# Optimization experiments

Measured on AMD Instinct MI355X. Metric: run time of the kernel, lower is better.

## Reference

```python
import jax, jax.numpy as jnp
import numpy as np

N_NODES = 50000
N_EDGES = 600000
IN_CH = 128
HID = 128
OUT_CH = 16
N_REL = 8
NEG_SLOPE = 0.2


def glorot(key, shape):
    fan_in, fan_out = shape[-2], shape[-1]
    lim = (6.0 / (fan_in + fan_out)) ** 0.5
    return jax.random.uniform(key, shape, jnp.float32, -lim, lim)


def setup_inputs() -> dict:
    key = jax.random.key(0)
    ks = jax.random.split(key, 16)
    x = jax.random.normal(ks[0], (N_NODES, IN_CH), jnp.float32)
    edge_index = jax.random.randint(ks[1], (2, N_EDGES), 0, N_NODES, jnp.int64)
    edge_type = jax.random.randint(ks[2], (N_EDGES,), 0, N_REL, jnp.int64)
    return {
        "x": x,
        "W1": glorot(ks[3], (N_REL, IN_CH, HID)),
        "q1": glorot(ks[4], (HID, 1)),
        "k1": glorot(ks[5], (HID, 1)),
        "b1": jnp.zeros((HID,), jnp.float32),
        "W2": glorot(ks[6], (N_REL, HID, HID)),
        "q2": glorot(ks[7], (HID, 1)),
        "k2": glorot(ks[8], (HID, 1)),
        "b2": jnp.zeros((HID,), jnp.float32),
        "lin_w": glorot(ks[9], (HID, OUT_CH)),
        "lin_b": jnp.zeros((OUT_CH,), jnp.float32),
        "edge_index": edge_index,
        "edge_type": edge_type,
    }


def rgat_conv(x, W, q, k, b, src, dst, etype, n_nodes):
    # Per-relation linear transform of all nodes: [R, N, H]
    xw = jnp.einsum('ni,rio->rno', x, W)
    hj = xw[etype, src]  # transformed source features per edge [E, H]
    hi = xw[etype, dst]  # transformed target features per edge [E, H]
    # additive self-attention logits (heads=1, dim=1): [E, 1]
    a = jax.nn.leaky_relu(hi @ q + hj @ k, NEG_SLOPE)
    # segment softmax over incoming edges of each target node (across-relation)
    amax = jax.ops.segment_max(a, dst, num_segments=n_nodes)  # [N, 1]
    e = jnp.exp(a - amax[dst])
    denom = jax.ops.segment_sum(e, dst, num_segments=n_nodes)  # [N, 1]
    alpha = e / denom[dst]
    # weighted scatter-add aggregation + bias
    out = jax.ops.segment_sum(alpha * hj, dst, num_segments=n_nodes)
    return out + b


def reference(x, W1, q1, k1, b1, W2, q2, k2, b2, lin_w, lin_b, edge_index, edge_type):
    src, dst = edge_index[0], edge_index[1]
    n = x.shape[0]
    h = jax.nn.relu(rgat_conv(x, W1, q1, k1, b1, src, dst, edge_type, n))
    h = jax.nn.relu(rgat_conv(h, W2, q2, k2, b2, src, dst, edge_type, n))
    h = h @ lin_w + lin_b                 # [N, out]
    g = jnp.mean(h, axis=0, keepdims=True)  # global_mean_pool -> [1, out]
    return jax.nn.log_softmax(g, axis=-1)
```

## Files before the change

kernel.cpp:

```cpp
#include <hip/hip_runtime.h>

#define CH 128
#define N_REL 8
#define OUT_CH 16
#define NEG_SLOPE 0.2f

typedef short short8 __attribute__((ext_vector_type(8)));
typedef float f32x4 __attribute__((ext_vector_type(4)));

__device__ __forceinline__ unsigned short f2bf(float f) {
    unsigned u = __float_as_uint(f);
    return (unsigned short)((u + 0x7fffu + ((u >> 16) & 1u)) >> 16);
}

__global__ void k_wqk(const float* __restrict__ W, const float* __restrict__ qv,
                      const float* __restrict__ kv, float* __restrict__ wq,
                      float* __restrict__ wk) {
    int r = blockIdx.x;
    int i = threadIdx.x;
    const float* row = W + ((size_t)r * CH + i) * CH;
    float aq = 0.f, ak = 0.f;
    for (int o = 0; o < CH; ++o) { float w = row[o]; aq += w * qv[o]; ak += w * kv[o]; }
    wq[r * CH + i] = aq;
    wk[r * CH + i] = ak;
}

__global__ void k_qkpack(const float* __restrict__ wq, const float* __restrict__ wk,
                         unsigned short* __restrict__ qkf) {
    int tid = threadIdx.x;
    int lane = tid & 63, ks = tid >> 6;
    int j = lane & 15, g = lane >> 4;
    const float* col = (j < 8) ? (wq + j * CH) : (wk + (j - 8) * CH);
    int k0 = ks * 32 + g * 8;
    unsigned pk[4];
    #pragma unroll
    for (int p = 0; p < 4; ++p) {
        unsigned lo = f2bf(col[k0 + 2 * p]);
        unsigned hi = f2bf(col[k0 + 2 * p + 1]);
        pk[p] = lo | (hi << 16);
    }
    *(uint4*)(qkf + (size_t)tid * 8) = make_uint4(pk[0], pk[1], pk[2], pk[3]);
}

__global__ __launch_bounds__(256) void k_sqsk2(const unsigned short* __restrict__ Xb,
                                               const unsigned short* __restrict__ qkf,
                                               float* __restrict__ sq,
                                               float* __restrict__ sk, int n) {
    const int wv = threadIdx.x >> 6, lane = threadIdx.x & 63;
    const int l15 = lane & 15, g = lane >> 4;
    const int t = blockIdx.x * 4 + wv;
    const int ntiles = (n + 15) >> 4;
    if (t >= ntiles) return;

    short8 qf[4];
    #pragma unroll
    for (int ks = 0; ks < 4; ++ks)
        qf[ks] = *(const short8*)(qkf + (size_t)(ks * 64 + lane) * 8);

    int row = t * 16 + l15;
    bool ok = row < n;
    int rowc = ok ? row : n - 1;
    const unsigned short* xrow = Xb + (size_t)rowc * CH + g * 8;
    short8 xf[4];
    #pragma unroll
    for (int ks = 0; ks < 4; ++ks) xf[ks] = *(const short8*)(xrow + ks * 32);

    f32x4 dq = {0.f, 0.f, 0.f, 0.f};
    #pragma unroll
    for (int ks = 0; ks < 4; ++ks)
        dq = __builtin_amdgcn_mfma_f32_16x16x32_bf16(qf[ks], xf[ks], dq, 0, 0, 0);

    if (ok) {
        float* base = (g < 2) ? sq : sk;
        int j0 = (g & 1) * 4;
        #pragma unroll
        for (int reg = 0; reg < 4; ++reg)
            base[(size_t)(j0 + reg) * n + row] = dq[reg];
    }
}

__global__ void k_cast(const float* __restrict__ X, unsigned short* __restrict__ Xb,
                       long total) {
    long i = ((long)blockIdx.x * 256 + threadIdx.x) * 8;
    if (i >= total) return;
    float4 v0 = *(const float4*)(X + i);
    float4 v1 = *(const float4*)(X + i + 4);
    ushort4 a, b;
    a.x = f2bf(v0.x); a.y = f2bf(v0.y); a.z = f2bf(v0.z); a.w = f2bf(v0.w);
    b.x = f2bf(v1.x); b.y = f2bf(v1.y); b.z = f2bf(v1.z); b.w = f2bf(v1.w);
    *(ushort4*)(Xb + i) = a;
    *(ushort4*)(Xb + i + 4) = b;
}

__global__ void k_wpack(const float* __restrict__ W, unsigned short* __restrict__ Wpk) {
    int t = blockIdx.x * 256 + threadIdx.x;
    if (t >= N_REL * 8 * 4 * 64) return;
    int lane = t & 63, ks = (t >> 6) & 3, ct = (t >> 8) & 7, r = t >> 11;
    int l15 = lane & 15, g = lane >> 4;
    const float* src = W + ((size_t)r * CH + ks * 32 + g * 8) * CH + ct * 16 + l15;
    unsigned pk[4];
    for (int p = 0; p < 4; ++p) {
        unsigned lo = f2bf(src[(2 * p) * CH]);
        unsigned hi = f2bf(src[(2 * p + 1) * CH]);
        pk[p] = lo | (hi << 16);
    }
    uint4 o = make_uint4(pk[0], pk[1], pk[2], pk[3]);
    *(uint4*)(Wpk + (size_t)t * 8) = o;
}

__global__ __launch_bounds__(256) void k_gemm3(const unsigned short* __restrict__ Xb,
                                               const unsigned short* __restrict__ Wpk,
                                               unsigned short* __restrict__ XW,
                                               int n, int nwaves) {
    const int wv = threadIdx.x >> 6, lane = threadIdx.x & 63;
    const int l15 = lane & 15, g = lane >> 4;
    const int w = blockIdx.x * 4 + wv;
    const int r = w & 7;
    const int slot = w >> 3;
    const int nslots = nwaves >> 3;
    const int ntiles = (n + 15) >> 4;

    short8 wf[8][4];
    const unsigned short* wr = Wpk + ((size_t)r * 32 * 64 + lane) * 8;
    #pragma unroll
    for (int ct = 0; ct < 8; ++ct)
        #pragma unroll
        for (int ks = 0; ks < 4; ++ks)
            wf[ct][ks] = *(const short8*)(wr + (size_t)(ct * 4 + ks) * 64 * 8);

    for (int t = slot; t < ntiles; t += nslots) {
        int row = t * 16 + l15;
        bool ok = row < n;
        int rowc = ok ? row : n - 1;
        const unsigned short* xrow = Xb + (size_t)rowc * CH + g * 8;
        short8 xf[4];
        #pragma unroll
        for (int ks = 0; ks < 4; ++ks) xf[ks] = *(const short8*)(xrow + ks * 32);
        unsigned short* orow = XW + ((size_t)r * n + row) * CH;
        #pragma unroll
        for (int ct = 0; ct < 8; ++ct) {
            f32x4 a = {0.f, 0.f, 0.f, 0.f};
            #pragma unroll
            for (int ks = 0; ks < 4; ++ks)
                a = __builtin_amdgcn_mfma_f32_16x16x32_bf16(wf[ct][ks], xf[ks], a, 0, 0, 0);
            unsigned p01, p23;
            asm("v_cvt_pk_bf16_f32 %0, %1, %2" : "=v"(p01) : "v"(a[0]), "v"(a[1]));
            asm("v_cvt_pk_bf16_f32 %0, %1, %2" : "=v"(p23) : "v"(a[2]), "v"(a[3]));
            if (ok) *(uint2*)(orow + ct * 16 + g * 4) = make_uint2(p01, p23);
        }
    }
}

__global__ void k_hist(const int* __restrict__ dst, int* __restrict__ count, int ne) {
    int e = blockIdx.x * 256 + threadIdx.x;
    if (e >= ne) return;
    atomicAdd(count + dst[e], 1);
}

__global__ __launch_bounds__(256) void k_scan1(const int* __restrict__ count,
                                               int* __restrict__ rowptr,
                                               int* __restrict__ bsum, int n) {
    __shared__ int wsum[4];
    int b = blockIdx.x, tid = threadIdx.x, lane = tid & 63, w = tid >> 6;
    int i0 = b * 1024 + tid * 4;
    int v0 = 0, v1 = 0, v2 = 0, v3 = 0;
    if (i0 + 3 < n) {
        int4 v = *(const int4*)(count + i0);
        v0 = v.x; v1 = v.y; v2 = v.z; v3 = v.w;
    } else {
        if (i0 < n) v0 = count[i0];
        if (i0 + 1 < n) v1 = count[i0 + 1];
        if (i0 + 2 < n) v2 = count[i0 + 2];
        if (i0 + 3 < n) v3 = count[i0 + 3];
    }
    int t1 = v0 + v1, t2 = t1 + v2, t3 = t2 + v3;
    int s = t3;
    #pragma unroll
    for (int off = 1; off < 64; off <<= 1) {
        int t = __shfl_up(s, off);
        if (lane >= off) s += t;
    }
    if (lane == 63) wsum[w] = s;
    __syncthreads();
    int wpre = 0;
    #pragma unroll
    for (int i = 0; i < 4; ++i) wpre += (i < w) ? wsum[i] : 0;
    int excl = wpre + s - t3;
    if (i0 < n) rowptr[i0] = excl;
    if (i0 + 1 < n) rowptr[i0 + 1] = excl + v0;
    if (i0 + 2 < n) rowptr[i0 + 2] = excl + t1;
    if (i0 + 3 < n) rowptr[i0 + 3] = excl + t2;
    if (tid == 0) bsum[b] = wsum[0] + wsum[1] + wsum[2] + wsum[3];
}

__global__ void k_scan2(int* __restrict__ bsum, int* __restrict__ total, int nb) {
    int lane = threadIdx.x;
    int carry = 0;
    for (int base = 0; base < nb; base += 64) {
        int i = base + lane;
        int v = (i < nb) ? bsum[i] : 0;
        int s = v;
        #pragma unroll
        for (int off = 1; off < 64; off <<= 1) {
            int t = __shfl_up(s, off);
            if (lane >= off) s += t;
        }
        if (i < nb) bsum[i] = carry + s - v;
        carry += __shfl(s, 63);
    }
    if (lane == 0) *total = carry;
}

__global__ __launch_bounds__(256) void k_scan3(int* __restrict__ rowptr,
                                               int* __restrict__ rowptr_work,
                                               const int* __restrict__ bsum,
                                               const int* __restrict__ total, int n) {
    int b = blockIdx.x;
    int i0 = b * 1024 + threadIdx.x * 4;
    int add = bsum[b];
    #pragma unroll
    for (int j = 0; j < 4; ++j) {
        int i = i0 + j;
        if (i < n) {
            int v = rowptr[i] + add;
            rowptr[i] = v;
            rowptr_work[i] = v;
        }
    }
    if (b == 0 && threadIdx.x == 0) rowptr[n] = *total;
}

__global__ void k_scatter(const int* __restrict__ src, const int* __restrict__ dst,
                          const int* __restrict__ et, int* __restrict__ rowptr_work,
                          int* __restrict__ pe, int ne) {
    int e = blockIdx.x * 256 + threadIdx.x;
    if (e >= ne) return;
    int pos = atomicAdd(rowptr_work + dst[e], 1);
    pe[pos] = (src[e] & 0xffff) | (et[e] << 16);
}

__global__ __launch_bounds__(256) void k_attn(
    const int* __restrict__ rowptr, const int* __restrict__ pe,
    const float* __restrict__ sq, const float* __restrict__ sk,
    const unsigned short* __restrict__ XW, const float* __restrict__ bias,
    unsigned short* __restrict__ outb, int n_nodes) {
    int wid = (blockIdx.x * 256 + threadIdx.x) >> 6;
    int lane = threadIdx.x & 63;
    if (wid >= n_nodes) return;
    const int l16 = lane & 15, g16 = lane >> 4;
    int r0 = rowptr[wid], r1 = rowptr[wid + 1];
    float acc[8] = {};
    float denom = 0.f;

    if (r1 > r0) {
        float sqv = (lane < N_REL) ? sq[lane * n_nodes + wid] : 0.f;

        float m = -1e30f;
        for (int c0 = r0; c0 < r1; c0 += 64) {
            int j = c0 + lane;
            float a = -1e30f;
            if (j < r1) {
                int p = pe[j];
                int s = p & 0xffff, t = p >> 16;
                float av = __shfl(sqv, t) + sk[t * n_nodes + s];
                a = av >= 0.f ? av : NEG_SLOPE * av;
            }
            m = fmaxf(m, a);
        }
        #pragma unroll
        for (int off = 32; off; off >>= 1) m = fmaxf(m, __shfl_xor(m, off));

        for (int c0 = r0; c0 < r1; c0 += 64) {
            int j = c0 + lane;
            float ev = 0.f;
            int p = 0;
            if (j < r1) {
                p = pe[j];
                int s = p & 0xffff, t = p >> 16;
                float av = __shfl(sqv, t) + sk[t * n_nodes + s];
                av = av >= 0.f ? av : NEG_SLOPE * av;
                ev = __expf(av - m);
            }
            float evs = ev;
            #pragma unroll
            for (int off = 32; off; off >>= 1) evs += __shfl_xor(evs, off);
            denom += evs;

            int C = r1 - c0;
            if (C > 64) C = 64;
            for (int jj = 0; jj < C; jj += 4) {
                int lsel = jj + g16;
                float evj = __shfl(ev, lsel);
                int pj = __shfl(p, lsel);
                int s = pj & 0xffff, t = pj >> 16;
                const unsigned short* row = XW + ((size_t)(t * n_nodes + s)) * CH + l16 * 8;
                uint4 v = *(const uint4*)row;
                acc[0] += evj * __uint_as_float(v.x << 16);
                acc[1] += evj * __uint_as_float(v.x & 0xffff0000u);
                acc[2] += evj * __uint_as_float(v.y << 16);
                acc[3] += evj * __uint_as_float(v.y & 0xffff0000u);
                acc[4] += evj * __uint_as_float(v.z << 16);
                acc[5] += evj * __uint_as_float(v.z & 0xffff0000u);
                acc[6] += evj * __uint_as_float(v.w << 16);
                acc[7] += evj * __uint_as_float(v.w & 0xffff0000u);
            }
        }
    }

    #pragma unroll
    for (int i = 0; i < 8; ++i) {
        acc[i] += __shfl_xor(acc[i], 16);
        acc[i] += __shfl_xor(acc[i], 32);
    }

    if (lane < 16) {
        float inv = denom > 0.f ? 1.f / denom : 0.f;
        unsigned pk[4];
        #pragma unroll
        for (int i = 0; i < 4; ++i) {
            float b0 = bias[l16 * 8 + 2 * i];
            float b1 = bias[l16 * 8 + 2 * i + 1];
            float o0 = acc[2 * i] * inv + b0;
            float o1 = acc[2 * i + 1] * inv + b1;
            o0 = o0 > 0.f ? o0 : 0.f;
            o1 = o1 > 0.f ? o1 : 0.f;
            pk[i] = (unsigned)f2bf(o0) | ((unsigned)f2bf(o1) << 16);
        }
        *(uint4*)(outb + (size_t)wid * CH + l16 * 8) = make_uint4(pk[0], pk[1], pk[2], pk[3]);
    }
}

__global__ __launch_bounds__(256) void k_colsum(const unsigned short* __restrict__ h,
                                                float* __restrict__ sum, int n_nodes) {
    __shared__ float cs[CH];
    int tid = threadIdx.x;
    int c2 = (tid & 63) * 2;
    int rw = tid >> 6;
    if (tid < CH) cs[tid] = 0.f;
    __syncthreads();
    float a0 = 0.f, a1 = 0.f;
    for (int row = blockIdx.x * 4 + rw; row < n_nodes; row += gridDim.x * 4) {
        unsigned v = *(const unsigned*)(h + (size_t)row * CH + c2);
        a0 += __uint_as_float(v << 16);
        a1 += __uint_as_float(v & 0xffff0000u);
    }
    atomicAdd(&cs[c2], a0);
    atomicAdd(&cs[c2 + 1], a1);
    __syncthreads();
    if (tid < CH) atomicAdd(sum + tid, cs[tid]);
}

__global__ void k_head(const float* __restrict__ sum, const float* __restrict__ lw,
                       const float* __restrict__ lb, float* __restrict__ outp, int n_nodes) {
    __shared__ float mean[CH];
    int t = threadIdx.x;
    mean[t] = sum[t] / (float)n_nodes;
    __syncthreads();
    if (t < OUT_CH) {
        float g = lb[t];
        for (int i = 0; i < CH; ++i) g += mean[i] * lw[i * OUT_CH + t];
        float m = g;
        #pragma unroll
        for (int off = 8; off; off >>= 1) m = fmaxf(m, __shfl_xor(m, off, 16));
        float ex = expf(g - m);
        float se = ex;
        #pragma unroll
        for (int off = 8; off; off >>= 1) se += __shfl_xor(se, off, 16);
        outp[t] = g - m - logf(se);
    }
}

extern "C" void kernel_launch(void* const* d_in, const int* in_sizes, int n_in,
                              void* d_out, int out_size, void* d_ws, size_t ws_size,
                              hipStream_t stream) {
    const float* x  = (const float*)d_in[0];
    const float* W1 = (const float*)d_in[1];
    const float* q1 = (const float*)d_in[2];
    const float* k1 = (const float*)d_in[3];
    const float* b1 = (const float*)d_in[4];
    const float* W2 = (const float*)d_in[5];
    const float* q2 = (const float*)d_in[6];
    const float* k2 = (const float*)d_in[7];
    const float* b2 = (const float*)d_in[8];
    const float* lw = (const float*)d_in[9];
    const float* lb = (const float*)d_in[10];
    const int* ei   = (const int*)d_in[11];
    const int* etp  = (const int*)d_in[12];

    const int n  = in_sizes[0] / CH;
    const int ne = in_sizes[12];
    const int* esrc = ei;
    const int* edst = ei + ne;

    char* ws = (char*)d_ws;
    size_t off = 0;
    auto carve = [&](size_t bytes) -> char* {
        char* p = ws + off;
        off = (off + bytes + 255) & ~(size_t)255;
        return p;
    };
    unsigned short* xw  = (unsigned short*)carve((size_t)N_REL * n * CH * 2);
    unsigned short* xb  = (unsigned short*)carve((size_t)n * CH * 2);
    unsigned short* h1b = (unsigned short*)carve((size_t)n * CH * 2);
    unsigned short* h2b = (unsigned short*)carve((size_t)n * CH * 2);
    unsigned short* wpk = (unsigned short*)carve((size_t)N_REL * 32 * 64 * 8 * 2);
    unsigned short* qkf = (unsigned short*)carve((size_t)256 * 8 * 2);
    float* sq     = (float*)carve((size_t)N_REL * n * 4);
    float* sk     = (float*)carve((size_t)N_REL * n * 4);
    float* wq     = (float*)carve(N_REL * CH * 4);
    float* wk     = (float*)carve(N_REL * CH * 4);
    int* count    = (int*)carve((size_t)n * 4);
    int* rowptr   = (int*)carve((size_t)(n + 1) * 4);
    int* rowptr_w = (int*)carve((size_t)n * 4);
    int* pe       = (int*)carve((size_t)ne * 4);
    int* bsum     = (int*)carve((size_t)256 * 4);
    int* total    = (int*)carve(4);
    float* sum128 = (float*)carve(CH * 4);

    hipMemsetAsync(count, 0, (size_t)n * 4, stream);
    hipMemsetAsync(sum128, 0, CH * 4, stream);

    const int nbscan = (n + 1023) / 1024;
    k_hist<<<(ne + 255) / 256, 256, 0, stream>>>(edst, count, ne);
    k_scan1<<<nbscan, 256, 0, stream>>>(count, rowptr, bsum, n);
    k_scan2<<<1, 64, 0, stream>>>(bsum, total, nbscan);
    k_scan3<<<nbscan, 256, 0, stream>>>(rowptr, rowptr_w, bsum, total, n);
    k_scatter<<<(ne + 255) / 256, 256, 0, stream>>>(esrc, edst, etp, rowptr_w, pe, ne);

    const int wpack_threads = N_REL * 8 * 4 * 64;
    const int NW = 2048;
    const int ntiles = (n + 15) >> 4;

    auto run_layer = [&](const unsigned short* Xb, const float* W, const float* qv,
                         const float* kv, const float* bv, unsigned short* houtb) {
        k_wqk<<<N_REL, CH, 0, stream>>>(W, qv, kv, wq, wk);
        k_wpack<<<(wpack_threads + 255) / 256, 256, 0, stream>>>(W, wpk);
        k_qkpack<<<1, 256, 0, stream>>>(wq, wk, qkf);
        k_gemm3<<<NW / 4, 256, 0, stream>>>(Xb, wpk, xw, n, NW);
        k_sqsk2<<<(ntiles + 3) / 4, 256, 0, stream>>>(Xb, qkf, sq, sk, n);
        k_attn<<<(n + 3) / 4, 256, 0, stream>>>(rowptr, pe, sq, sk, xw, bv, houtb, n);
    };

    k_cast<<<(int)(((long)n * CH / 8 + 255) / 256), 256, 0, stream>>>(x, xb, (long)n * CH);
    run_layer(xb, W1, q1, k1, b1, h1b);
    run_layer(h1b, W2, q2, k2, b2, h2b);

    k_colsum<<<256, 256, 0, stream>>>(h2b, sum128, n);
    k_head<<<1, CH, 0, stream>>>(sum128, lw, lb, (float*)d_out, n);
}
```

Baseline: 282.7 us.

## Horizontally fuse independent prep, scan, GEMM and scatter kernels into fewer launches

Independent kernels are merged into combined launches that pick their role from the block index: cast with histogram, scan1 with the first layer's W·q/W·k, scan2 with weight packing, and GEMM with the sq/sk projection and edge scatter. The second layer's W·q/W·k is also folded into the first layer's attention launch. This cuts the number of launches and the serialization gaps between small kernels, and lets small jobs overlap with large ones. The cost is more complex launch-dependency reasoning and mixed-role blocks that may raise register pressure or hurt occupancy in the fused kernels.

```diff
diff --git a/kernel.cpp b/kernel.cpp
--- a/kernel.cpp
+++ b/kernel.cpp
@@ -13,11 +13,28 @@
     return (unsigned short)((u + 0x7fffu + ((u >> 16) & 1u)) >> 16);
 }
 
-__global__ void k_wqk(const float* __restrict__ W, const float* __restrict__ qv,
-                      const float* __restrict__ kv, float* __restrict__ wq,
-                      float* __restrict__ wk) {
-    int r = blockIdx.x;
-    int i = threadIdx.x;
+
+__device__ __forceinline__ void dev_cast(const float* __restrict__ X,
+                                         unsigned short* __restrict__ Xb,
+                                         long total, int b, int tid) {
+    long i = ((long)b * 256 + tid) * 8;
+    if (i >= total) return;
+    float4 v0 = *(const float4*)(X + i);
+    float4 v1 = *(const float4*)(X + i + 4);
+    ushort4 a, c;
+    a.x = f2bf(v0.x); a.y = f2bf(v0.y); a.z = f2bf(v0.z); a.w = f2bf(v0.w);
+    c.x = f2bf(v1.x); c.y = f2bf(v1.y); c.z = f2bf(v1.z); c.w = f2bf(v1.w);
+    *(ushort4*)(Xb + i) = a;
+    *(ushort4*)(Xb + i + 4) = c;
+}
+
+__device__ __forceinline__ void dev_wqk(const float* __restrict__ W,
+                                        const float* __restrict__ qv,
+                                        const float* __restrict__ kv,
+                                        float* __restrict__ wq, float* __restrict__ wk,
+                                        int rb, int tid) {
+    int r = rb * 2 + (tid >> 7);
+    int i = tid & 127;
     const float* row = W + ((size_t)r * CH + i) * CH;
     float aq = 0.f, ak = 0.f;
     for (int o = 0; o < CH; ++o) { float w = row[o]; aq += w * qv[o]; ak += w * kv[o]; }
@@ -25,9 +42,24 @@
     wk[r * CH + i] = ak;
 }
 
-__global__ void k_qkpack(const float* __restrict__ wq, const float* __restrict__ wk,
-                         unsigned short* __restrict__ qkf) {
-    int tid = threadIdx.x;
+__device__ __forceinline__ void dev_wpack(const float* __restrict__ W,
+                                          unsigned short* __restrict__ Wpk, int t) {
+    int lane = t & 63, ks = (t >> 6) & 3, ct = (t >> 8) & 7, r = t >> 11;
+    int l15 = lane & 15, g = lane >> 4;
+    const float* src = W + ((size_t)r * CH + ks * 32 + g * 8) * CH + ct * 16 + l15;
+    unsigned pk[4];
+    #pragma unroll
+    for (int p = 0; p < 4; ++p) {
+        unsigned lo = f2bf(src[(2 * p) * CH]);
+        unsigned hi = f2bf(src[(2 * p + 1) * CH]);
+        pk[p] = lo | (hi << 16);
+    }
+    *(uint4*)(Wpk + (size_t)t * 8) = make_uint4(pk[0], pk[1], pk[2], pk[3]);
+}
+
+__device__ __forceinline__ void dev_qkpack(const float* __restrict__ wq,
+                                           const float* __restrict__ wk,
+                                           unsigned short* __restrict__ qkf, int tid) {
     int lane = tid & 63, ks = tid >> 6;
     int j = lane & 15, g = lane >> 4;
     const float* col = (j < 8) ? (wq + j * CH) : (wk + (j - 8) * CH);
@@ -42,126 +74,31 @@
     *(uint4*)(qkf + (size_t)tid * 8) = make_uint4(pk[0], pk[1], pk[2], pk[3]);
 }
 
-__global__ __launch_bounds__(256) void k_sqsk2(const unsigned short* __restrict__ Xb,
-                                               const unsigned short* __restrict__ qkf,
-                                               float* __restrict__ sq,
-                                               float* __restrict__ sk, int n) {
-    const int wv = threadIdx.x >> 6, lane = threadIdx.x & 63;
-    const int l15 = lane & 15, g = lane >> 4;
-    const int t = blockIdx.x * 4 + wv;
-    const int ntiles = (n + 15) >> 4;
-    if (t >= ntiles) return;
-
-    short8 qf[4];
-    #pragma unroll
-    for (int ks = 0; ks < 4; ++ks)
-        qf[ks] = *(const short8*)(qkf + (size_t)(ks * 64 + lane) * 8);
-
-    int row = t * 16 + l15;
-    bool ok = row < n;
-    int rowc = ok ? row : n - 1;
-    const unsigned short* xrow = Xb + (size_t)rowc * CH + g * 8;
-    short8 xf[4];
-    #pragma unroll
-    for (int ks = 0; ks < 4; ++ks) xf[ks] = *(const short8*)(xrow + ks * 32);
-
-    f32x4 dq = {0.f, 0.f, 0.f, 0.f};
-    #pragma unroll
-    for (int ks = 0; ks < 4; ++ks)
-        dq = __builtin_amdgcn_mfma_f32_16x16x32_bf16(qf[ks], xf[ks], dq, 0, 0, 0);
-
-    if (ok) {
-        float* base = (g < 2) ? sq : sk;
-        int j0 = (g & 1) * 4;
-        #pragma unroll
-        for (int reg = 0; reg < 4; ++reg)
-            base[(size_t)(j0 + reg) * n + row] = dq[reg];
-    }
-}
-
-__global__ void k_cast(const float* __restrict__ X, unsigned short* __restrict__ Xb,
-                       long total) {
-    long i = ((long)blockIdx.x * 256 + threadIdx.x) * 8;
-    if (i >= total) return;
-    float4 v0 = *(const float4*)(X + i);
-    float4 v1 = *(const float4*)(X + i + 4);
-    ushort4 a, b;
-    a.x = f2bf(v0.x); a.y = f2bf(v0.y); a.z = f2bf(v0.z); a.w = f2bf(v0.w);
-    b.x = f2bf(v1.x); b.y = f2bf(v1.y); b.z = f2bf(v1.z); b.w = f2bf(v1.w);
-    *(ushort4*)(Xb + i) = a;
-    *(ushort4*)(Xb + i + 4) = b;
-}
-
-__global__ void k_wpack(const float* __restrict__ W, unsigned short* __restrict__ Wpk) {
-    int t = blockIdx.x * 256 + threadIdx.x;
-    if (t >= N_REL * 8 * 4 * 64) return;
-    int lane = t & 63, ks = (t >> 6) & 3, ct = (t >> 8) & 7, r = t >> 11;
-    int l15 = lane & 15, g = lane >> 4;
-    const float* src = W + ((size_t)r * CH + ks * 32 + g * 8) * CH + ct * 16 + l15;
-    unsigned pk[4];
-    for (int p = 0; p < 4; ++p) {
-        unsigned lo = f2bf(src[(2 * p) * CH]);
-        unsigned hi = f2bf(src[(2 * p + 1) * CH]);
-        pk[p] = lo | (hi << 16);
-    }
-    uint4 o = make_uint4(pk[0], pk[1], pk[2], pk[3]);
-    *(uint4*)(Wpk + (size_t)t * 8) = o;
-}
-
-__global__ __launch_bounds__(256) void k_gemm3(const unsigned short* __restrict__ Xb,
-                                               const unsigned short* __restrict__ Wpk,
-                                               unsigned short* __restrict__ XW,
-                                               int n, int nwaves) {
-    const int wv = threadIdx.x >> 6, lane = threadIdx.x & 63;
-    const int l15 = lane & 15, g = lane >> 4;
-    const int w = blockIdx.x * 4 + wv;
-    const int r = w & 7;
-    const int slot = w >> 3;
-    const int nslots = nwaves >> 3;
-    const int ntiles = (n + 15) >> 4;
-
-    short8 wf[8][4];
-    const unsigned short* wr = Wpk + ((size_t)r * 32 * 64 + lane) * 8;
-    #pragma unroll
-    for (int ct = 0; ct < 8; ++ct)
-        #pragma unroll
-        for (int ks = 0; ks < 4; ++ks)
-            wf[ct][ks] = *(const short8*)(wr + (size_t)(ct * 4 + ks) * 64 * 8);
-
-    for (int t = slot; t < ntiles; t += nslots) {
-        int row = t * 16 + l15;
-        bool ok = row < n;
-        int rowc = ok ? row : n - 1;
-        const unsigned short* xrow = Xb + (size_t)rowc * CH + g * 8;
-        short8 xf[4];
-        #pragma unroll
-        for (int ks = 0; ks < 4; ++ks) xf[ks] = *(const short8*)(xrow + ks * 32);
-        unsigned short* orow = XW + ((size_t)r * n + row) * CH;
-        #pragma unroll
-        for (int ct = 0; ct < 8; ++ct) {
-            f32x4 a = {0.f, 0.f, 0.f, 0.f};
-            #pragma unroll
-            for (int ks = 0; ks < 4; ++ks)
-                a = __builtin_amdgcn_mfma_f32_16x16x32_bf16(wf[ct][ks], xf[ks], a, 0, 0, 0);
-            unsigned p01, p23;
-            asm("v_cvt_pk_bf16_f32 %0, %1, %2" : "=v"(p01) : "v"(a[0]), "v"(a[1]));
-            asm("v_cvt_pk_bf16_f32 %0, %1, %2" : "=v"(p23) : "v"(a[2]), "v"(a[3]));
-            if (ok) *(uint2*)(orow + ct * 16 + g * 4) = make_uint2(p01, p23);
-        }
-    }
-}
-
-__global__ void k_hist(const int* __restrict__ dst, int* __restrict__ count, int ne) {
-    int e = blockIdx.x * 256 + threadIdx.x;
-    if (e >= ne) return;
-    atomicAdd(count + dst[e], 1);
-}
-
-__global__ __launch_bounds__(256) void k_scan1(const int* __restrict__ count,
-                                               int* __restrict__ rowptr,
-                                               int* __restrict__ bsum, int n) {
+
+__global__ void k_cast_hist(const float* __restrict__ X, unsigned short* __restrict__ Xb,
+                            long total, const int* __restrict__ dst,
+                            int* __restrict__ count, int ne, int nb_cast) {
+    int b = blockIdx.x, tid = threadIdx.x;
+    if (b < nb_cast) {
+        dev_cast(X, Xb, total, b, tid);
+    } else {
+        int e = (b - nb_cast) * 256 + tid;
+        if (e < ne) atomicAdd(count + dst[e], 1);
+    }
+}
+
+__global__ __launch_bounds__(256) void k_scan1_wqk(const int* __restrict__ count,
+                                                   int* __restrict__ rowptr,
+                                                   int* __restrict__ bsum, int n, int nbscan,
+                                                   const float* __restrict__ W,
+                                                   const float* __restrict__ qv,
+                                                   const float* __restrict__ kv,
+                                                   float* __restrict__ wq,
+                                                   float* __restrict__ wk) {
+    int b = blockIdx.x, tid = threadIdx.x;
+    if (b >= nbscan) { dev_wqk(W, qv, kv, wq, wk, b - nbscan, tid); return; }
     __shared__ int wsum[4];
-    int b = blockIdx.x, tid = threadIdx.x, lane = tid & 63, w = tid >> 6;
+    int lane = tid & 63, w = tid >> 6;
     int i0 = b * 1024 + tid * 4;
     int v0 = 0, v1 = 0, v2 = 0, v3 = 0;
     if (i0 + 3 < n) {
@@ -193,22 +130,36 @@
     if (tid == 0) bsum[b] = wsum[0] + wsum[1] + wsum[2] + wsum[3];
 }
 
-__global__ void k_scan2(int* __restrict__ bsum, int* __restrict__ total, int nb) {
-    int lane = threadIdx.x;
-    int carry = 0;
-    for (int base = 0; base < nb; base += 64) {
-        int i = base + lane;
-        int v = (i < nb) ? bsum[i] : 0;
-        int s = v;
-        #pragma unroll
-        for (int off = 1; off < 64; off <<= 1) {
-            int t = __shfl_up(s, off);
-            if (lane >= off) s += t;
-        }
-        if (i < nb) bsum[i] = carry + s - v;
-        carry += __shfl(s, 63);
-    }
-    if (lane == 0) *total = carry;
+__global__ __launch_bounds__(256) void k_scan2_wprep(int* __restrict__ bsum,
+                                                     int* __restrict__ total, int nb,
+                                                     const float* __restrict__ W,
+                                                     unsigned short* __restrict__ Wpk,
+                                                     const float* __restrict__ wq,
+                                                     const float* __restrict__ wk,
+                                                     unsigned short* __restrict__ qkf) {
+    int b = blockIdx.x, tid = threadIdx.x;
+    if (b == 0) {
+        if (tid >= 64) return;
+        int lane = tid;
+        int carry = 0;
+        for (int base = 0; base < nb; base += 64) {
+            int i = base + lane;
+            int v = (i < nb) ? bsum[i] : 0;
+            int s = v;
+            #pragma unroll
+            for (int off = 1; off < 64; off <<= 1) {
+                int t = __shfl_up(s, off);
+                if (lane >= off) s += t;
+            }
+            if (i < nb) bsum[i] = carry + s - v;
+            carry += __shfl(s, 63);
+        }
+        if (lane == 0) *total = carry;
+    } else if (b <= 64) {
+        dev_wpack(W, Wpk, (b - 1) * 256 + tid);
+    } else {
+        dev_qkpack(wq, wk, qkf, tid);
+    }
 }
 
 __global__ __launch_bounds__(256) void k_scan3(int* __restrict__ rowptr,
@@ -230,21 +181,100 @@
     if (b == 0 && threadIdx.x == 0) rowptr[n] = *total;
 }
 
-__global__ void k_scatter(const int* __restrict__ src, const int* __restrict__ dst,
-                          const int* __restrict__ et, int* __restrict__ rowptr_work,
-                          int* __restrict__ pe, int ne) {
-    int e = blockIdx.x * 256 + threadIdx.x;
-    if (e >= ne) return;
-    int pos = atomicAdd(rowptr_work + dst[e], 1);
-    pe[pos] = (src[e] & 0xffff) | (et[e] << 16);
-}
-
-__global__ __launch_bounds__(256) void k_attn(
+
+__global__ __launch_bounds__(256) void k_fat(
+    const unsigned short* __restrict__ Xb, const unsigned short* __restrict__ Wpk,
+    const unsigned short* __restrict__ qkf, unsigned short* __restrict__ XW,
+    float* __restrict__ sq, float* __restrict__ sk, int n, int nwaves,
+    int nb_gemm, int nb_sqsk,
+    const int* __restrict__ esrc, const int* __restrict__ edst,
+    const int* __restrict__ etp, int* __restrict__ rowptr_work,
+    int* __restrict__ pe, int ne) {
+    const int b = blockIdx.x, tid = threadIdx.x;
+    const int wv = tid >> 6, lane = tid & 63;
+    const int l15 = lane & 15, g = lane >> 4;
+    const int ntiles = (n + 15) >> 4;
+
+    if (b < nb_gemm) {
+        const int w = b * 4 + wv;
+        const int r = w & 7;
+        const int slot = w >> 3;
+        const int nslots = nwaves >> 3;
+
+        short8 wf[8][4];
+        const unsigned short* wr = Wpk + ((size_t)r * 32 * 64 + lane) * 8;
+        #pragma unroll
+        for (int ct = 0; ct < 8; ++ct)
+            #pragma unroll
+            for (int ks = 0; ks < 4; ++ks)
+                wf[ct][ks] = *(const short8*)(wr + (size_t)(ct * 4 + ks) * 64 * 8);
+
+        for (int t = slot; t < ntiles; t += nslots) {
+            int row = t * 16 + l15;
+            bool ok = row < n;
+            int rowc = ok ? row : n - 1;
+            const unsigned short* xrow = Xb + (size_t)rowc * CH + g * 8;
+            short8 xf[4];
+            #pragma unroll
+            for (int ks = 0; ks < 4; ++ks) xf[ks] = *(const short8*)(xrow + ks * 32);
+            unsigned short* orow = XW + ((size_t)r * n + row) * CH;
+            #pragma unroll
+            for (int ct = 0; ct < 8; ++ct) {
+                f32x4 a = {0.f, 0.f, 0.f, 0.f};
+                #pragma unroll
+                for (int ks = 0; ks < 4; ++ks)
+                    a = __builtin_amdgcn_mfma_f32_16x16x32_bf16(wf[ct][ks], xf[ks], a, 0, 0, 0);
+                unsigned p01, p23;
+                asm("v_cvt_pk_bf16_f32 %0, %1, %2" : "=v"(p01) : "v"(a[0]), "v"(a[1]));
+                asm("v_cvt_pk_bf16_f32 %0, %1, %2" : "=v"(p23) : "v"(a[2]), "v"(a[3]));
+                if (ok) *(uint2*)(orow + ct * 16 + g * 4) = make_uint2(p01, p23);
+            }
+        }
+    } else if (b < nb_gemm + nb_sqsk) {
+        const int t = (b - nb_gemm) * 4 + wv;
+        if (t >= ntiles) return;
+        short8 qf[4];
+        #pragma unroll
+        for (int ks = 0; ks < 4; ++ks)
+            qf[ks] = *(const short8*)(qkf + (size_t)(ks * 64 + lane) * 8);
+        int row = t * 16 + l15;
+        bool ok = row < n;
+        int rowc = ok ? row : n - 1;
+        const unsigned short* xrow = Xb + (size_t)rowc * CH + g * 8;
+        short8 xf[4];
+        #pragma unroll
+        for (int ks = 0; ks < 4; ++ks) xf[ks] = *(const short8*)(xrow + ks * 32);
+        f32x4 dq = {0.f, 0.f, 0.f, 0.f};
+        #pragma unroll
+        for (int ks = 0; ks < 4; ++ks)
+            dq = __builtin_amdgcn_mfma_f32_16x16x32_bf16(qf[ks], xf[ks], dq, 0, 0, 0);
+        if (ok) {
+            float* base = (g < 2) ? sq : sk;
+            int j0 = (g & 1) * 4;
+            #pragma unroll
+            for (int reg = 0; reg < 4; ++reg)
+                base[(size_t)(j0 + reg) * n + row] = dq[reg];
+        }
+    } else {
+        int e = (b - nb_gemm - nb_sqsk) * 256 + tid;
+        if (e >= ne) return;
+        int pos = atomicAdd(rowptr_work + edst[e], 1);
+        pe[pos] = (esrc[e] & 0xffff) | (etp[e] << 16);
+    }
+}
+
+
+__global__ __launch_bounds__(256) void k_attn_wqk(
     const int* __restrict__ rowptr, const int* __restrict__ pe,
     const float* __restrict__ sq, const float* __restrict__ sk,
     const unsigned short* __restrict__ XW, const float* __restrict__ bias,
-    unsigned short* __restrict__ outb, int n_nodes) {
-    int wid = (blockIdx.x * 256 + threadIdx.x) >> 6;
+    unsigned short* __restrict__ outb, int n_nodes,
+    const float* __restrict__ Wn, const float* __restrict__ qn,
+    const float* __restrict__ kn, float* __restrict__ wqn,
+    float* __restrict__ wkn, int nb_wqk) {
+    int b = blockIdx.x;
+    if (b < nb_wqk) { dev_wqk(Wn, qn, kn, wqn, wkn, b, threadIdx.x); return; }
+    int wid = ((b - nb_wqk) * 256 + threadIdx.x) >> 6;
     int lane = threadIdx.x & 63;
     if (wid >= n_nodes) return;
     const int l16 = lane & 15, g16 = lane >> 4;
@@ -329,6 +359,18 @@
         *(uint4*)(outb + (size_t)wid * CH + l16 * 8) = make_uint4(pk[0], pk[1], pk[2], pk[3]);
     }
 }
+
+
+__global__ __launch_bounds__(256) void k_wprep2(const float* __restrict__ W,
+                                                unsigned short* __restrict__ Wpk,
+                                                const float* __restrict__ wq,
+                                                const float* __restrict__ wk,
+                                                unsigned short* __restrict__ qkf) {
+    int b = blockIdx.x, tid = threadIdx.x;
+    if (b < 64) dev_wpack(W, Wpk, b * 256 + tid);
+    else dev_qkpack(wq, wk, qkf, tid);
+}
+
 
 __global__ __launch_bounds__(256) void k_colsum(const unsigned short* __restrict__ h,
                                                 float* __restrict__ sum, int n_nodes) {
@@ -421,29 +463,32 @@
     hipMemsetAsync(sum128, 0, CH * 4, stream);
 
     const int nbscan = (n + 1023) / 1024;
-    k_hist<<<(ne + 255) / 256, 256, 0, stream>>>(edst, count, ne);
-    k_scan1<<<nbscan, 256, 0, stream>>>(count, rowptr, bsum, n);
-    k_scan2<<<1, 64, 0, stream>>>(bsum, total, nbscan);
+    const int nb_cast = (int)(((long)n * CH / 8 + 255) / 256);
+    const int nb_hist = (ne + 255) / 256;
+    const int NW = 2048;
+    const int nb_gemm = NW / 4;
+    const int ntiles = (n + 15) >> 4;
+    const int nb_sqsk = (ntiles + 3) / 4;
+    const int nb_scat = (ne + 255) / 256;
+    const int nb_attn = (n + 3) / 4;
+
+    k_cast_hist<<<nb_cast + nb_hist, 256, 0, stream>>>(x, xb, (long)n * CH, edst, count, ne, nb_cast);
+    k_scan1_wqk<<<nbscan + 4, 256, 0, stream>>>(count, rowptr, bsum, n, nbscan, W1, q1, k1, wq, wk);
+    k_scan2_wprep<<<66, 256, 0, stream>>>(bsum, total, nbscan, W1, wpk, wq, wk, qkf);
     k_scan3<<<nbscan, 256, 0, stream>>>(rowptr, rowptr_w, bsum, total, n);
-    k_scatter<<<(ne + 255) / 256, 256, 0, stream>>>(esrc, edst, etp, rowptr_w, pe, ne);
-
-    const int wpack_threads = N_REL * 8 * 4 * 64;
-    const int NW = 2048;
-    const int ntiles = (n + 15) >> 4;
-
-    auto run_layer = [&](const unsigned short* Xb, const float* W, const float* qv,
-                         const float* kv, const float* bv, unsigned short* houtb) {
-        k_wqk<<<N_REL, CH, 0, stream>>>(W, qv, kv, wq, wk);
-        k_wpack<<<(wpack_threads + 255) / 256, 256, 0, stream>>>(W, wpk);
-        k_qkpack<<<1, 256, 0, stream>>>(wq, wk, qkf);
-        k_gemm3<<<NW / 4, 256, 0, stream>>>(Xb, wpk, xw, n, NW);
-        k_sqsk2<<<(ntiles + 3) / 4, 256, 0, stream>>>(Xb, qkf, sq, sk, n);
-        k_attn<<<(n + 3) / 4, 256, 0, stream>>>(rowptr, pe, sq, sk, xw, bv, houtb, n);
-    };
-
-    k_cast<<<(int)(((long)n * CH / 8 + 255) / 256), 256, 0, stream>>>(x, xb, (long)n * CH);
-    run_layer(xb, W1, q1, k1, b1, h1b);
-    run_layer(h1b, W2, q2, k2, b2, h2b);
+    k_fat<<<nb_gemm + nb_sqsk + nb_scat, 256, 0, stream>>>(xb, wpk, qkf, xw, sq, sk, n, NW,
+                                                           nb_gemm, nb_sqsk,
+                                                           esrc, edst, etp, rowptr_w, pe, ne);
+    k_attn_wqk<<<4 + nb_attn, 256, 0, stream>>>(rowptr, pe, sq, sk, xw, b1, h1b, n,
+                                                W2, q2, k2, wq, wk, 4);
+    k_wprep2<<<65, 256, 0, stream>>>(W2, wpk, wq, wk, qkf);
+    k_fat<<<nb_gemm + nb_sqsk, 256, 0, stream>>>(h1b, wpk, qkf, xw, sq, sk, n, NW,
+                                                 nb_gemm, nb_sqsk,
+                                                 esrc, edst, etp, rowptr_w, pe, 0);
+    k_attn_wqk<<<nb_attn, 256, 0, stream>>>(rowptr, pe, sq, sk, xw, b2, h2b, n,
+                                            (const float*)nullptr, (const float*)nullptr,
+                                            (const float*)nullptr, (float*)nullptr,
+                                            (float*)nullptr, 0);
 
     k_colsum<<<256, 256, 0, stream>>>(h2b, sum128, n);
     k_head<<<1, CH, 0, stream>>>(sum128, lw, lb, (float*)d_out, n);
```

New measurement: 254.2 us. 1.11x faster.
